# Optimization experiments

Hardware: AMD Instinct MI355X
Metric: run time of the kernel (lower is better)

The kernel has to match this reference:

```python
import jax, jax.numpy as jnp
import numpy as np
import math

B, LQ, LK = 1024, 1, 1024
LQD, SQD, H = 256, 128, 2
HD = SQD // H  # 64
EPS = 1e-6


def _ln(x, g, b):
    mu = x.mean(-1, keepdims=True)
    var = ((x - mu) ** 2).mean(-1, keepdims=True)
    return (x - mu) / jnp.sqrt(var + EPS) * g + b


def setup_inputs() -> dict:
    key = jax.random.key(0)
    ks = jax.random.split(key, 16)
    w = lambda k, s: jax.random.normal(k, s, jnp.float32) * 0.02
    return {
        "q_feats": jax.random.normal(ks[0], (B, LQ, LQD), jnp.float32),
        "k_feats": jax.random.normal(ks[1], (B, LK, SQD), jnp.float32),
        "msk": jax.random.randint(ks[2], (B, LK), 0, 2).astype(jnp.int32),
        "ln1_g": jnp.ones(LQD), "ln1_b": jnp.zeros(LQD),
        "W1": w(ks[3], (LQD, SQD)), "b1": jnp.zeros(SQD),
        "lnq_g": jnp.ones(SQD), "lnq_b": jnp.zeros(SQD),
        "lnk_g": jnp.ones(SQD), "lnk_b": jnp.zeros(SQD),
        "Wq": w(ks[4], (SQD, SQD)), "bq": jnp.zeros(SQD),
        "Wk": w(ks[5], (SQD, SQD)), "bk": jnp.zeros(SQD),
        "Wv": w(ks[6], (SQD, SQD)), "bv": jnp.zeros(SQD),
        "Wo": w(ks[7], (SQD, SQD)), "bo": jnp.zeros(SQD),
        "scale_w": jax.random.uniform(ks[8], (SQD,), jnp.float32, 0.01, 2.0),
        "ln2_g": jnp.ones(SQD), "ln2_b": jnp.zeros(SQD),
        "W2": w(ks[9], (SQD, LQD)), "b2": jnp.zeros(LQD),
    }


def reference(q_feats, k_feats, msk, ln1_g, ln1_b, W1, b1, lnq_g, lnq_b,
              lnk_g, lnk_b, Wq, bq, Wk, bk, Wv, bv, Wo, bo, scale_w,
              ln2_g, ln2_b, W2, b2):
    gelu = lambda x: jax.nn.gelu(x, approximate=False)
    # q_block1: LN -> Linear -> GELU (dropout = identity in eval)
    q_atten = gelu(_ln(q_feats, ln1_g, ln1_b) @ W1 + b1)  # [B,LQ,SQD]
    kv_in = _ln(k_feats, lnk_g, lnk_b)                     # [B,LK,SQD]
    q_in = _ln(q_atten, lnq_g, lnq_b)
    # masked self-attention
    qh = (q_in @ Wq + bq).reshape(B, LQ, H, HD).transpose(0, 2, 1, 3)
    kh = (kv_in @ Wk + bk).reshape(B, LK, H, HD).transpose(0, 2, 1, 3)
    vh = (kv_in @ Wv + bv).reshape(B, LK, H, HD).transpose(0, 2, 1, 3)
    scores = jnp.einsum('bhqd,bhkd->bhqk', qh, kh) / math.sqrt(HD)
    m = msk.astype(scores.dtype)[:, None, None, :]  # [B,1,1,LK]
    scores = jnp.where(m == 0, -1e9, scores * m)
    attn = jax.nn.softmax(scores, axis=-1)
    ctx = jnp.einsum('bhqk,bhkd->bhqd', attn, vh)
    ctx = ctx.transpose(0, 2, 1, 3).reshape(B, LQ, SQD)
    attn_out = gelu(ctx @ Wo + bo)
    q_atten = q_atten + attn_out
    # scaled broadcast residual into k_feats
    scaled = jnp.swapaxes(q_atten * scale_w, 0, 1)         # [LQ,B,SQD]
    k_out = k_feats + jnp.tile(scaled, (B, 1, 1))          # [B,B,SQD]
    # q_block2
    q_out = q_feats + gelu(_ln(q_atten, ln2_g, ln2_b) @ W2 + b2)
    return (q_out, k_out)
```

## Files before the change

### kernel.cpp

```cpp
#include <hip/hip_runtime.h>
#include <math.h>

#define B_    1024
#define LK_   1024
#define LQD_  256
#define SQD_  128
#define EPSLN 1e-6f
#define LOG2E 1.4426950408889634f

__device__ __forceinline__ float gelu_exact(float x) {
    return 0.5f * x * (1.0f + erff(x * 0.70710678118654752f));
}

__global__ __launch_bounds__(256, 4)
void fused_q_attn_kernel(
    const float* __restrict__ q_feats, const float* __restrict__ k_feats,
    const int*   __restrict__ msk,
    const float* __restrict__ ln1_g, const float* __restrict__ ln1_b,
    const float* __restrict__ W1,    const float* __restrict__ b1,
    const float* __restrict__ lnq_g, const float* __restrict__ lnq_b,
    const float* __restrict__ lnk_g, const float* __restrict__ lnk_b,
    const float* __restrict__ Wq,    const float* __restrict__ bq,
    const float* __restrict__ Wk,    const float* __restrict__ bk,
    const float* __restrict__ Wv,    const float* __restrict__ bv,
    const float* __restrict__ Wo,    const float* __restrict__ bo,
    const float* __restrict__ scale_w,
    const float* __restrict__ ln2_g, const float* __restrict__ ln2_b,
    const float* __restrict__ W2,    const float* __restrict__ b2,
    float* __restrict__ q_out, float* __restrict__ sc_ws)
{
    const int b    = blockIdx.x;
    const int tid  = threadIdx.x;
    const int wave = tid >> 6;
    const int lane = tid & 63;

    __shared__ float s_qn[256];
    __shared__ float s_q1[128];
    __shared__ float s_qi[128];
    __shared__ float s_qh[128];
    __shared__ float s_u[2][128];
    __shared__ float s_c[2];
    __shared__ float s_red[8];
    __shared__ int   s_idx[4][256];
    __shared__ float s_w[4][2][128];
    __shared__ float s_ml[4][2][2];
    __shared__ float s_wn[2][128];
    __shared__ float s_ctx[128];
    __shared__ float s_qa[128];
    __shared__ float s_qn2[128];

    float x = q_feats[b * LQD_ + tid];
    float rs = x, rss = x * x;
    #pragma unroll
    for (int o = 32; o >= 1; o >>= 1) { rs += __shfl_xor(rs, o); rss += __shfl_xor(rss, o); }
    if (lane == 0) { s_red[wave * 2] = rs; s_red[wave * 2 + 1] = rss; }
    __syncthreads();
    {
        float sum  = s_red[0] + s_red[2] + s_red[4] + s_red[6];
        float ssum = s_red[1] + s_red[3] + s_red[5] + s_red[7];
        float mu   = sum * (1.0f / 256.0f);
        float var  = ssum * (1.0f / 256.0f) - mu * mu;
        float rstd = rsqrtf(var + EPSLN);
        s_qn[tid] = (x - mu) * rstd * ln1_g[tid] + ln1_b[tid];
    }
    __syncthreads();

    if (tid < 128) {
        float acc = b1[tid];
        for (int c = 0; c < 256; ++c) acc = fmaf(s_qn[c], W1[c * 128 + tid], acc);
        s_q1[tid] = gelu_exact(acc);
    }
    __syncthreads();

    float v1 = (tid < 128) ? s_q1[tid] : 0.0f;
    rs = v1; rss = v1 * v1;
    #pragma unroll
    for (int o = 32; o >= 1; o >>= 1) { rs += __shfl_xor(rs, o); rss += __shfl_xor(rss, o); }
    __syncthreads();
    if (lane == 0) { s_red[wave * 2] = rs; s_red[wave * 2 + 1] = rss; }
    __syncthreads();
    {
        float sum  = s_red[0] + s_red[2] + s_red[4] + s_red[6];
        float ssum = s_red[1] + s_red[3] + s_red[5] + s_red[7];
        float mu   = sum * (1.0f / 128.0f);
        float var  = ssum * (1.0f / 128.0f) - mu * mu;
        float rstd = rsqrtf(var + EPSLN);
        if (tid < 128) s_qi[tid] = (v1 - mu) * rstd * lnq_g[tid] + lnq_b[tid];
    }
    __syncthreads();

    if (tid < 128) {
        float acc = bq[tid];
        for (int c = 0; c < 128; ++c) acc = fmaf(s_qi[c], Wq[c * 128 + tid], acc);
        s_qh[tid] = acc;
    }
    __syncthreads();

    const float SCL = 0.125f * LOG2E;
    if (tid < 128) {
        float a0 = 0.f, a1 = 0.f;
        for (int e = 0; e < 64; ++e) {
            a0 = fmaf(Wk[tid * 128 + e],      s_qh[e],      a0);
            a1 = fmaf(Wk[tid * 128 + 64 + e], s_qh[64 + e], a1);
        }
        s_u[0][tid] = a0 * SCL;
        s_u[1][tid] = a1 * SCL;
    }
    if (tid == 0) { float a = 0.f; for (int e = 0; e < 64; ++e) a = fmaf(bk[e],      s_qh[e],      a); s_c[0] = a * SCL; }
    if (tid == 1) { float a = 0.f; for (int e = 0; e < 64; ++e) a = fmaf(bk[64 + e], s_qh[64 + e], a); s_c[1] = a * SCL; }

    const int* mrow = msk + b * LK_;
    int cnt = 0;
    #pragma unroll
    for (int i = 0; i < 4; ++i) {
        int r = (wave << 8) + (i << 6) + lane;
        int mk = mrow[r];
        unsigned long long bal = __ballot(mk != 0);
        int pre = __popcll(bal & ((1ull << lane) - 1ull));
        if (mk) s_idx[wave][cnt + pre] = r;
        cnt += __popcll(bal);
    }
    __syncthreads();

    const int  c0i = lane * 2, c1i = lane * 2 + 1;
    const float g0  = lnk_g[c0i], g1  = lnk_g[c1i];
    const float hb0 = lnk_b[c0i], hb1 = lnk_b[c1i];
    const float u00 = s_u[0][c0i], u01 = s_u[0][c1i];
    const float u10 = s_u[1][c0i], u11 = s_u[1][c1i];
    const float cc0 = s_c[0],      cc1 = s_c[1];

    const float2* kf2 = (const float2*)(k_feats) + (size_t)b * (LK_ * (SQD_ / 2));

    float m0 = -1e30f, l0 = 0.f, w00 = 0.f, w01 = 0.f;
    float m1 = -1e30f, l1 = 0.f, w10 = 0.f, w11 = 0.f;

    float2 xv = make_float2(0.f, 0.f);
    if (cnt > 0) xv = kf2[s_idx[wave][0] * 64 + lane];
    for (int t = 0; t < cnt; ++t) {
        float2 xn = make_float2(0.f, 0.f);
        if (t + 1 < cnt) xn = kf2[s_idx[wave][t + 1] * 64 + lane];

        float a = xv.x + xv.y;
        float q = xv.x * xv.x + xv.y * xv.y;
        #pragma unroll
        for (int o = 32; o >= 1; o >>= 1) { a += __shfl_xor(a, o); q += __shfl_xor(q, o); }
        float mu2 = a * (1.f / 128.f);
        float vr  = q * (1.f / 128.f) - mu2 * mu2;
        float rs2 = rsqrtf(vr + EPSLN);
        float kv0 = (xv.x - mu2) * rs2 * g0 + hb0;
        float kv1 = (xv.y - mu2) * rs2 * g1 + hb1;

        float p0 = kv0 * u00 + kv1 * u01;
        float p1 = kv0 * u10 + kv1 * u11;
        #pragma unroll
        for (int o = 32; o >= 1; o >>= 1) { p0 += __shfl_xor(p0, o); p1 += __shfl_xor(p1, o); }
        float sc0 = p0 + cc0, sc1 = p1 + cc1;

        float mn0 = fmaxf(m0, sc0);
        float cr0 = exp2f(m0 - mn0);
        float pp0 = exp2f(sc0 - mn0);
        m0 = mn0; l0 = l0 * cr0 + pp0;
        w00 = w00 * cr0 + pp0 * kv0;
        w01 = w01 * cr0 + pp0 * kv1;
        float mn1 = fmaxf(m1, sc1);
        float cr1 = exp2f(m1 - mn1);
        float pp1 = exp2f(sc1 - mn1);
        m1 = mn1; l1 = l1 * cr1 + pp1;
        w10 = w10 * cr1 + pp1 * kv0;
        w11 = w11 * cr1 + pp1 * kv1;

        xv = xn;
    }

    s_w[wave][0][c0i] = w00; s_w[wave][0][c1i] = w01;
    s_w[wave][1][c0i] = w10; s_w[wave][1][c1i] = w11;
    if (lane == 0) {
        s_ml[wave][0][0] = m0; s_ml[wave][0][1] = l0;
        s_ml[wave][1][0] = m1; s_ml[wave][1][1] = l1;
    }
    __syncthreads();

    if (tid < 128) {
        #pragma unroll
        for (int h = 0; h < 2; ++h) {
            float mg = fmaxf(fmaxf(s_ml[0][h][0], s_ml[1][h][0]),
                             fmaxf(s_ml[2][h][0], s_ml[3][h][0]));
            float lt = 0.f, wt = 0.f;
            #pragma unroll
            for (int wv = 0; wv < 4; ++wv) {
                float e = exp2f(s_ml[wv][h][0] - mg);
                lt += s_ml[wv][h][1] * e;
                wt += s_w[wv][h][tid] * e;
            }
            s_wn[h][tid] = wt / lt;
        }
    }
    __syncthreads();

    if (tid < 128) {
        int h = tid >> 6;
        float acc = bv[tid];
        for (int c = 0; c < 128; ++c) acc = fmaf(s_wn[h][c], Wv[c * 128 + tid], acc);
        s_ctx[tid] = acc;
    }
    __syncthreads();

    if (tid < 128) {
        float acc = bo[tid];
        for (int c = 0; c < 128; ++c) acc = fmaf(s_ctx[c], Wo[c * 128 + tid], acc);
        float qa = s_q1[tid] + gelu_exact(acc);
        s_qa[tid] = qa;
        sc_ws[b * 128 + tid] = qa * scale_w[tid];
    }
    __syncthreads();

    float v2 = (tid < 128) ? s_qa[tid] : 0.0f;
    rs = v2; rss = v2 * v2;
    #pragma unroll
    for (int o = 32; o >= 1; o >>= 1) { rs += __shfl_xor(rs, o); rss += __shfl_xor(rss, o); }
    __syncthreads();
    if (lane == 0) { s_red[wave * 2] = rs; s_red[wave * 2 + 1] = rss; }
    __syncthreads();
    {
        float sum  = s_red[0] + s_red[2] + s_red[4] + s_red[6];
        float ssum = s_red[1] + s_red[3] + s_red[5] + s_red[7];
        float mu   = sum * (1.0f / 128.0f);
        float var  = ssum * (1.0f / 128.0f) - mu * mu;
        float rstd = rsqrtf(var + EPSLN);
        if (tid < 128) s_qn2[tid] = (v2 - mu) * rstd * ln2_g[tid] + ln2_b[tid];
    }
    __syncthreads();

    {
        float acc = b2[tid];
        for (int c = 0; c < 128; ++c) acc = fmaf(s_qn2[c], W2[c * 256 + tid], acc);
        q_out[b * LQD_ + tid] = q_feats[b * LQD_ + tid] + gelu_exact(acc);
    }
}

__global__ __launch_bounds__(256)
void kout_kernel(const float4* __restrict__ kf,
                 const float4* __restrict__ sc,
                 float4* __restrict__ out)
{
    const int total4 = B_ * LK_ * (SQD_ / 4);
    const int stride = gridDim.x * blockDim.x;
    for (int idx = blockIdx.x * blockDim.x + threadIdx.x; idx < total4; idx += stride) {
        float4 k = kf[idx];
        int j = (idx >> 5) & (LK_ - 1);
        float4 s = sc[(j << 5) + (idx & 31)];
        float4 o;
        o.x = k.x + s.x; o.y = k.y + s.y; o.z = k.z + s.z; o.w = k.w + s.w;
        out[idx] = o;
    }
}

extern "C" void kernel_launch(void* const* d_in, const int* in_sizes, int n_in,
                              void* d_out, int out_size, void* d_ws, size_t ws_size,
                              hipStream_t stream)
{
    (void)in_sizes; (void)n_in; (void)out_size; (void)ws_size;
    const float* q_feats = (const float*)d_in[0];
    const float* k_feats = (const float*)d_in[1];
    const int*   msk     = (const int*)d_in[2];
    const float* ln1_g   = (const float*)d_in[3];
    const float* ln1_b   = (const float*)d_in[4];
    const float* W1      = (const float*)d_in[5];
    const float* b1      = (const float*)d_in[6];
    const float* lnq_g   = (const float*)d_in[7];
    const float* lnq_b   = (const float*)d_in[8];
    const float* lnk_g   = (const float*)d_in[9];
    const float* lnk_b   = (const float*)d_in[10];
    const float* Wq      = (const float*)d_in[11];
    const float* bq      = (const float*)d_in[12];
    const float* Wk      = (const float*)d_in[13];
    const float* bk      = (const float*)d_in[14];
    const float* Wv      = (const float*)d_in[15];
    const float* bv      = (const float*)d_in[16];
    const float* Wo      = (const float*)d_in[17];
    const float* bo      = (const float*)d_in[18];
    const float* scale_w = (const float*)d_in[19];
    const float* ln2_g   = (const float*)d_in[20];
    const float* ln2_b   = (const float*)d_in[21];
    const float* W2      = (const float*)d_in[22];
    const float* b2      = (const float*)d_in[23];

    float* q_out = (float*)d_out;
    float* k_out = (float*)d_out + (size_t)B_ * LQD_;
    float* sc_ws = (float*)d_ws;

    fused_q_attn_kernel<<<B_, 256, 0, stream>>>(
        q_feats, k_feats, msk, ln1_g, ln1_b, W1, b1, lnq_g, lnq_b,
        lnk_g, lnk_b, Wq, bq, Wk, bk, Wv, bv, Wo, bo, scale_w,
        ln2_g, ln2_b, W2, b2, q_out, sc_ws);

    kout_kernel<<<2048, 256, 0, stream>>>(
        (const float4*)k_feats, (const float4*)sc_ws, (float4*)k_out);
}
```

Baseline: 419.2 us.

## Fuse k_out broadcast into attention kernel and restructure masked-row loop

```diff
diff --git a/kernel.cpp b/kernel.cpp
--- a/kernel.cpp
+++ b/kernel.cpp
@@ -13,7 +13,7 @@
 }
 
 __global__ __launch_bounds__(256, 4)
-void fused_q_attn_kernel(
+void fused_joint_kernel(
     const float* __restrict__ q_feats, const float* __restrict__ k_feats,
     const int*   __restrict__ msk,
     const float* __restrict__ ln1_g, const float* __restrict__ ln1_b,
@@ -27,7 +27,7 @@
     const float* __restrict__ scale_w,
     const float* __restrict__ ln2_g, const float* __restrict__ ln2_b,
     const float* __restrict__ W2,    const float* __restrict__ b2,
-    float* __restrict__ q_out, float* __restrict__ sc_ws)
+    float* __restrict__ q_out, float* __restrict__ k_out)
 {
     const int b    = blockIdx.x;
     const int tid  = threadIdx.x;
@@ -48,6 +48,7 @@
     __shared__ float s_ctx[128];
     __shared__ float s_qa[128];
     __shared__ float s_qn2[128];
+    __shared__ float s_sc[128];
 
     float x = q_feats[b * LQD_ + tid];
     float rs = x, rss = x * x;
@@ -67,6 +68,7 @@
 
     if (tid < 128) {
         float acc = b1[tid];
+        #pragma unroll 4
         for (int c = 0; c < 256; ++c) acc = fmaf(s_qn[c], W1[c * 128 + tid], acc);
         s_q1[tid] = gelu_exact(acc);
     }
@@ -91,6 +93,7 @@
 
     if (tid < 128) {
         float acc = bq[tid];
+        #pragma unroll 4
         for (int c = 0; c < 128; ++c) acc = fmaf(s_qi[c], Wq[c * 128 + tid], acc);
         s_qh[tid] = acc;
     }
@@ -99,6 +102,7 @@
     const float SCL = 0.125f * LOG2E;
     if (tid < 128) {
         float a0 = 0.f, a1 = 0.f;
+        #pragma unroll 4
         for (int e = 0; e < 64; ++e) {
             a0 = fmaf(Wk[tid * 128 + e],      s_qh[e],      a0);
             a1 = fmaf(Wk[tid * 128 + 64 + e], s_qh[64 + e], a1);
@@ -129,48 +133,79 @@
     const float u10 = s_u[1][c0i], u11 = s_u[1][c1i];
     const float cc0 = s_c[0],      cc1 = s_c[1];
 
+    const float gu00 = g0 * u00, gu01 = g1 * u01;
+    const float gu10 = g0 * u10, gu11 = g1 * u11;
+    float sgu0 = gu00 + gu01;
+    float sgu1 = gu10 + gu11;
+    float dd0  = fmaf(hb0, u00, hb1 * u01);
+    float dd1  = fmaf(hb0, u10, hb1 * u11);
+    #pragma unroll
+    for (int o = 32; o >= 1; o >>= 1) {
+        sgu0 += __shfl_xor(sgu0, o); sgu1 += __shfl_xor(sgu1, o);
+        dd0  += __shfl_xor(dd0,  o); dd1  += __shfl_xor(dd1,  o);
+    }
+    const float d0 = dd0 + cc0, d1 = dd1 + cc1;
+
     const float2* kf2 = (const float2*)(k_feats) + (size_t)b * (LK_ * (SQD_ / 2));
 
     float m0 = -1e30f, l0 = 0.f, w00 = 0.f, w01 = 0.f;
     float m1 = -1e30f, l1 = 0.f, w10 = 0.f, w11 = 0.f;
 
-    float2 xv = make_float2(0.f, 0.f);
-    if (cnt > 0) xv = kf2[s_idx[wave][0] * 64 + lane];
-    for (int t = 0; t < cnt; ++t) {
-        float2 xn = make_float2(0.f, 0.f);
-        if (t + 1 < cnt) xn = kf2[s_idx[wave][t + 1] * 64 + lane];
-
-        float a = xv.x + xv.y;
-        float q = xv.x * xv.x + xv.y * xv.y;
-        #pragma unroll
-        for (int o = 32; o >= 1; o >>= 1) { a += __shfl_xor(a, o); q += __shfl_xor(q, o); }
-        float mu2 = a * (1.f / 128.f);
-        float vr  = q * (1.f / 128.f) - mu2 * mu2;
-        float rs2 = rsqrtf(vr + EPSLN);
-        float kv0 = (xv.x - mu2) * rs2 * g0 + hb0;
-        float kv1 = (xv.y - mu2) * rs2 * g1 + hb1;
-
-        float p0 = kv0 * u00 + kv1 * u01;
-        float p1 = kv0 * u10 + kv1 * u11;
-        #pragma unroll
-        for (int o = 32; o >= 1; o >>= 1) { p0 += __shfl_xor(p0, o); p1 += __shfl_xor(p1, o); }
-        float sc0 = p0 + cc0, sc1 = p1 + cc1;
-
-        float mn0 = fmaxf(m0, sc0);
-        float cr0 = exp2f(m0 - mn0);
-        float pp0 = exp2f(sc0 - mn0);
-        m0 = mn0; l0 = l0 * cr0 + pp0;
-        w00 = w00 * cr0 + pp0 * kv0;
-        w01 = w01 * cr0 + pp0 * kv1;
-        float mn1 = fmaxf(m1, sc1);
-        float cr1 = exp2f(m1 - mn1);
-        float pp1 = exp2f(sc1 - mn1);
-        m1 = mn1; l1 = l1 * cr1 + pp1;
-        w10 = w10 * cr1 + pp1 * kv0;
-        w11 = w11 * cr1 + pp1 * kv1;
-
-        xv = xn;
-    }
+    #define ROW_STEP(xx, valid)                                               \
+    {                                                                         \
+        float a_  = xx.x + xx.y;                                              \
+        float q_  = fmaf(xx.x, xx.x, xx.y * xx.y);                            \
+        float p0_ = fmaf(xx.x, gu00, xx.y * gu01);                            \
+        float p1_ = fmaf(xx.x, gu10, xx.y * gu11);                            \
+        _Pragma("unroll")                                                     \
+        for (int o_ = 32; o_ >= 1; o_ >>= 1) {                                \
+            a_  += __shfl_xor(a_,  o_); q_  += __shfl_xor(q_,  o_);           \
+            p0_ += __shfl_xor(p0_, o_); p1_ += __shfl_xor(p1_, o_);           \
+        }                                                                     \
+        if (valid) {                                                          \
+            float mu_   = a_ * (1.f / 128.f);                                 \
+            float var_  = q_ * (1.f / 128.f) - mu_ * mu_;                     \
+            float rstd_ = rsqrtf(var_ + EPSLN);                               \
+            float sc0_  = fmaf(rstd_, p0_ - mu_ * sgu0, d0);                  \
+            float sc1_  = fmaf(rstd_, p1_ - mu_ * sgu1, d1);                  \
+            float kv0_  = fmaf((xx.x - mu_) * rstd_, g0, hb0);                \
+            float kv1_  = fmaf((xx.y - mu_) * rstd_, g1, hb1);                \
+            float mn0_  = fmaxf(m0, sc0_);                                    \
+            float cr0_  = exp2f(m0 - mn0_);                                   \
+            float pp0_  = exp2f(sc0_ - mn0_);                                 \
+            m0 = mn0_; l0 = fmaf(l0, cr0_, pp0_);                             \
+            w00 = fmaf(w00, cr0_, pp0_ * kv0_);                               \
+            w01 = fmaf(w01, cr0_, pp0_ * kv1_);                               \
+            float mn1_  = fmaxf(m1, sc1_);                                    \
+            float cr1_  = exp2f(m1 - mn1_);                                   \
+            float pp1_  = exp2f(sc1_ - mn1_);                                 \
+            m1 = mn1_; l1 = fmaf(l1, cr1_, pp1_);                             \
+            w10 = fmaf(w10, cr1_, pp1_ * kv0_);                               \
+            w11 = fmaf(w11, cr1_, pp1_ * kv1_);                               \
+        }                                                                     \
+    }
+
+    float2 xr0 = make_float2(0.f, 0.f), xr1 = xr0, xr2 = xr0, xr3 = xr0;
+    if (0 < cnt) xr0 = kf2[s_idx[wave][0] * 64 + lane];
+    if (1 < cnt) xr1 = kf2[s_idx[wave][1] * 64 + lane];
+    if (2 < cnt) xr2 = kf2[s_idx[wave][2] * 64 + lane];
+    if (3 < cnt) xr3 = kf2[s_idx[wave][3] * 64 + lane];
+
+    for (int t = 0; t < cnt; t += 4) {
+        float2 xn0 = make_float2(0.f, 0.f), xn1 = xn0, xn2 = xn0, xn3 = xn0;
+        if (t + 4 < cnt) xn0 = kf2[s_idx[wave][t + 4] * 64 + lane];
+        if (t + 5 < cnt) xn1 = kf2[s_idx[wave][t + 5] * 64 + lane];
+        if (t + 6 < cnt) xn2 = kf2[s_idx[wave][t + 6] * 64 + lane];
+        if (t + 7 < cnt) xn3 = kf2[s_idx[wave][t + 7] * 64 + lane];
+
+        ROW_STEP(xr0, true);
+        ROW_STEP(xr1, (t + 1) < cnt);
+        ROW_STEP(xr2, (t + 2) < cnt);
+        ROW_STEP(xr3, (t + 3) < cnt);
+
+        xr0 = xn0; xr1 = xn1; xr2 = xn2; xr3 = xn3;
+    }
+    #undef ROW_STEP
 
     s_w[wave][0][c0i] = w00; s_w[wave][0][c1i] = w01;
     s_w[wave][1][c0i] = w10; s_w[wave][1][c1i] = w11;
@@ -200,6 +235,7 @@
     if (tid < 128) {
         int h = tid >> 6;
         float acc = bv[tid];
+        #pragma unroll 4
         for (int c = 0; c < 128; ++c) acc = fmaf(s_wn[h][c], Wv[c * 128 + tid], acc);
         s_ctx[tid] = acc;
     }
@@ -207,10 +243,11 @@
 
     if (tid < 128) {
         float acc = bo[tid];
+        #pragma unroll 4
         for (int c = 0; c < 128; ++c) acc = fmaf(s_ctx[c], Wo[c * 128 + tid], acc);
         float qa = s_q1[tid] + gelu_exact(acc);
         s_qa[tid] = qa;
-        sc_ws[b * 128 + tid] = qa * scale_w[tid];
+        s_sc[tid] = qa * scale_w[tid];
     }
     __syncthreads();
 
@@ -233,25 +270,25 @@
 
     {
         float acc = b2[tid];
+        #pragma unroll 4
         for (int c = 0; c < 128; ++c) acc = fmaf(s_qn2[c], W2[c * 256 + tid], acc);
         q_out[b * LQD_ + tid] = q_feats[b * LQD_ + tid] + gelu_exact(acc);
     }
-}
-
-__global__ __launch_bounds__(256)
-void kout_kernel(const float4* __restrict__ kf,
-                 const float4* __restrict__ sc,
-                 float4* __restrict__ out)
-{
-    const int total4 = B_ * LK_ * (SQD_ / 4);
-    const int stride = gridDim.x * blockDim.x;
-    for (int idx = blockIdx.x * blockDim.x + threadIdx.x; idx < total4; idx += stride) {
-        float4 k = kf[idx];
-        int j = (idx >> 5) & (LK_ - 1);
-        float4 s = sc[(j << 5) + (idx & 31)];
-        float4 o;
-        o.x = k.x + s.x; o.y = k.y + s.y; o.z = k.z + s.z; o.w = k.w + s.w;
-        out[idx] = o;
+
+    {
+        const int c4 = tid & 31;
+        const int r0 = tid >> 5;
+        const float4 sv = ((const float4*)s_sc)[c4];
+        const size_t colbase = (size_t)b * 32 + c4;
+        const float4* __restrict__ kin4  = (const float4*)k_feats;
+        float4*       __restrict__ kout4 = (float4*)k_out;
+        #pragma unroll 4
+        for (int b2 = r0; b2 < B_; b2 += 8) {
+            size_t o = (size_t)b2 * (LK_ * 32) + colbase;
+            float4 kx = kin4[o];
+            float4 ov = make_float4(kx.x + sv.x, kx.y + sv.y, kx.z + sv.z, kx.w + sv.w);
+            kout4[o] = ov;
+        }
     }
 }
 
@@ -259,7 +296,7 @@
                               void* d_out, int out_size, void* d_ws, size_t ws_size,
                               hipStream_t stream)
 {
-    (void)in_sizes; (void)n_in; (void)out_size; (void)ws_size;
+    (void)in_sizes; (void)n_in; (void)out_size; (void)d_ws; (void)ws_size;
     const float* q_feats = (const float*)d_in[0];
     const float* k_feats = (const float*)d_in[1];
     const int*   msk     = (const int*)d_in[2];
@@ -287,13 +324,9 @@
 
     float* q_out = (float*)d_out;
     float* k_out = (float*)d_out + (size_t)B_ * LQD_;
-    float* sc_ws = (float*)d_ws;
-
-    fused_q_attn_kernel<<<B_, 256, 0, stream>>>(
+
+    fused_joint_kernel<<<B_, 256, 0, stream>>>(
         q_feats, k_feats, msk, ln1_g, ln1_b, W1, b1, lnq_g, lnq_b,
         lnk_g, lnk_b, Wq, bq, Wk, bk, Wv, bv, Wo, bo, scale_w,
-        ln2_g, ln2_b, W2, b2, q_out, sc_ws);
-
-    kout_kernel<<<2048, 256, 0, stream>>>(
-        (const float4*)k_feats, (const float4*)sc_ws, (float4*)k_out);
+        ln2_g, ln2_b, W2, b2, q_out, k_out);
 }
```

New measurement: 387.0 us. 7.7% less time.
